# Kernel optimization log

Hardware: AMD Instinct MI355X
Metric: run time of the kernel (lower is better)

## Reference

```python
import jax, jax.numpy as jnp
import numpy as np

B, N_PER, C, KG, KTOP, KNN = 8, 2048, 256, 16, 512, 32
N = B * N_PER
E = N * KG
EPS = 1e-5


def setup_inputs() -> dict:
    key = jax.random.key(0)
    ks = jax.random.split(key, 32)
    s = 0.05
    x = jax.random.normal(ks[0], (N, C), jnp.float32)
    x_origin = jax.random.normal(ks[1], (N, C), jnp.float32)
    xyz = jax.random.uniform(ks[2], (N, 3), jnp.float32)
    # graph: every node is a dst with KG incoming edges from random nodes of the SAME sample
    edge_dst = jnp.repeat(jnp.arange(N, dtype=jnp.int32), KG)
    src_local = jax.random.randint(ks[3], (E,), 0, N_PER, dtype=jnp.int32)
    edge_src = src_local + (edge_dst // N_PER) * N_PER
    # EdgeConv params (theta on x_j - x_i, phi on x_i)
    theta_w = jax.random.normal(ks[4], (C, C), jnp.float32) * s
    theta_b = jax.random.normal(ks[5], (C,), jnp.float32) * s
    phi_w = jax.random.normal(ks[6], (C, C), jnp.float32) * s
    phi_b = jax.random.normal(ks[7], (C,), jnp.float32) * s
    # region_score_mlp: Conv1d(C,64,1)-ReLU-BN(64)-Conv1d(64,32,1)-ReLU-BN(32)-Conv1d(32,1,1)
    w1 = jax.random.normal(ks[8], (64, C), jnp.float32) * s
    b1 = jax.random.normal(ks[9], (64,), jnp.float32) * s
    g1 = 1.0 + 0.1 * jax.random.normal(ks[10], (64,), jnp.float32)
    be1 = 0.1 * jax.random.normal(ks[11], (64,), jnp.float32)
    m1 = 0.1 * jax.random.normal(ks[12], (64,), jnp.float32)
    v1 = jax.random.uniform(ks[13], (64,), jnp.float32, 0.5, 1.5)
    w2 = jax.random.normal(ks[14], (32, 64), jnp.float32) * s
    b2 = jax.random.normal(ks[15], (32,), jnp.float32) * s
    g2 = 1.0 + 0.1 * jax.random.normal(ks[16], (32,), jnp.float32)
    be2 = 0.1 * jax.random.normal(ks[17], (32,), jnp.float32)
    m2 = 0.1 * jax.random.normal(ks[18], (32,), jnp.float32)
    v2 = jax.random.uniform(ks[19], (32,), jnp.float32, 0.5, 1.5)
    w3 = jax.random.normal(ks[20], (1, 32), jnp.float32) * s
    b3 = jax.random.normal(ks[21], (1,), jnp.float32) * s
    return dict(x=x, x_origin=x_origin, xyz=xyz, edge_src=edge_src, edge_dst=edge_dst,
                theta_w=theta_w, theta_b=theta_b, phi_w=phi_w, phi_b=phi_b,
                w1=w1, b1=b1, g1=g1, be1=be1, m1=m1, v1=v1,
                w2=w2, b2=b2, g2=g2, be2=be2, m2=m2, v2=v2, w3=w3, b3=b3)


def _bn(t, g, b, m, v):
    return (t - m) * jax.lax.rsqrt(v + EPS) * g + b


def _forward(x, x_origin, xyz, edge_src, edge_dst,
             theta_w, theta_b, phi_w, phi_b,
             w1, b1, g1, be1, m1, v1, w2, b2, g2, be2, m2, v2, w3, b3):
    # EdgeConv: h_i = max_{j->i}( theta(x_j - x_i) + phi(x_i) ), then residual add
    msg = ((x[edge_src] - x[edge_dst]) @ theta_w.T + theta_b
           + x[edge_dst] @ phi_w.T + phi_b)                      # [E, C]
    h = jax.ops.segment_max(msg, edge_dst, num_segments=N)       # [N, C]
    x1 = h + x                                                   # residual
    # per-node MLP (Conv1d kernel-size 1 == linear), BN in eval mode
    t = _bn(jax.nn.relu(x1 @ w1.T + b1), g1, be1, m1, v1)
    t = _bn(jax.nn.relu(t @ w2.T + b2), g2, be2, m2, v2)
    score = t @ w3.T + b3                                        # [N, 1]
    score_b = score.reshape(B, N_PER)                            # vps_score
    # per-batch top-k (cls=False path: select by raw score, descending)
    topk_vals, topk_idx = jax.lax.top_k(score_b, KTOP)           # [B, KTOP]
    perm = (topk_idx + jnp.arange(B, dtype=topk_idx.dtype)[:, None] * N_PER).reshape(-1)
    x_new = x1[perm].reshape(B, KTOP, C)
    x_copy = x_origin[perm].reshape(B, KTOP, -1)
    xyz_sel = xyz[perm].reshape(B, KTOP, 3)
    # rebuild 32-NN graph per sample on selected points (batched, no per-b python calls)
    d2 = jnp.sum((xyz_sel[:, :, None, :] - xyz_sel[:, None, :, :]) ** 2, axis=-1)  # [B,K,K]
    _, knn_idx = jax.lax.top_k(-d2, KNN)                         # [B, KTOP, 32]
    return knn_idx, x_new, x_copy, score_b, topk_vals


def reference(x, x_origin, xyz, edge_src, edge_dst,
              theta_w, theta_b, phi_w, phi_b,
              w1, b1, g1, be1, m1, v1, w2, b2, g2, be2, m2, v2, w3, b3):
    return _forward(x, x_origin, xyz, edge_src, edge_dst,
                    theta_w, theta_b, phi_w, phi_b,
                    w1, b1, g1, be1, m1, v1, w2, b2, g2, be2, m2, v2, w3, b3)
```

## Files before the change

### kernel.cpp

```cpp
#include <hip/hip_runtime.h>
#include <math.h>

constexpr int B     = 8;
constexpr int N_PER = 2048;
constexpr int C     = 256;
constexpr int KG    = 16;
constexpr int KTOP  = 512;
constexpr int KNN   = 32;
constexpr int N     = B * N_PER;
constexpr float EPS = 1e-5f;

typedef __attribute__((ext_vector_type(8))) short  short8;
typedef __attribute__((ext_vector_type(4))) float  f32x4;

__device__ inline void split3(float f, unsigned short& h, unsigned short& m,
                              unsigned short& l)
{
    const unsigned u  = __float_as_uint(f);
    const unsigned r1 = (u + 0x7FFFu + ((u >> 16) & 1u)) & 0xFFFF0000u;
    h = (unsigned short)(r1 >> 16);
    const float f2 = f - __uint_as_float(r1);
    const unsigned u2 = __float_as_uint(f2);
    const unsigned r2 = (u2 + 0x7FFFu + ((u2 >> 16) & 1u)) & 0xFFFF0000u;
    m = (unsigned short)(r2 >> 16);
    const float f3 = f2 - __uint_as_float(r2);
    const unsigned u3 = __float_as_uint(f3);
    l = (unsigned short)((u3 + 0x7FFFu + ((u3 >> 16) & 1u)) >> 16);
}

__device__ inline void cvt_store24(unsigned short* dh, unsigned short* dm,
                                   unsigned short* dl, float4 a, float4 b)
{
    short8 h, m, l;
    unsigned short hh, mm, ll;
    float v[8] = {a.x, a.y, a.z, a.w, b.x, b.y, b.z, b.w};
#pragma unroll
    for (int j = 0; j < 8; ++j) {
        split3(v[j], hh, mm, ll);
        h[j] = (short)hh;
        m[j] = (short)mm;
        l[j] = (short)ll;
    }
    *(short8*)dh = h;
    *(short8*)dm = m;
    *(short8*)dl = l;
}

__device__ inline void split8v(const float* __restrict__ s,
                               unsigned short* __restrict__ dh,
                               unsigned short* __restrict__ dm,
                               unsigned short* __restrict__ dl)
{
    float4 a = *(const float4*)s;
    float4 b = *(const float4*)(s + 4);
    float v[8] = {a.x, a.y, a.z, a.w, b.x, b.y, b.z, b.w};
    short8 h8, m8, l8;
    unsigned short hh, mm, ll;
#pragma unroll
    for (int j = 0; j < 8; ++j) {
        split3(v[j], hh, mm, ll);
        h8[j] = (short)hh;
        m8[j] = (short)mm;
        l8[j] = (short)ll;
    }
    *(short8*)dh = h8;
    *(short8*)dm = m8;
    *(short8*)dl = l8;
}

constexpr int GW = C * C / 8;

__global__ __launch_bounds__(256) void k0w_split(
    const float* __restrict__ thw, const float* __restrict__ phw,
    unsigned short* __restrict__ th, unsigned short* __restrict__ tm,
    unsigned short* __restrict__ tl,
    unsigned short* __restrict__ ph, unsigned short* __restrict__ pm,
    unsigned short* __restrict__ pl)
{
    const int g = blockIdx.x * 256 + threadIdx.x;
    if (g < GW) {
        const int o = g * 8;
        split8v(thw + o, th + o, tm + o, tl + o);
    } else if (g < 2 * GW) {
        const int o = (g - GW) * 8;
        split8v(phw + o, ph + o, pm + o, pl + o);
    }
}

__global__ __launch_bounds__(256) void k1_wp(
    const float* __restrict__ x,
    const unsigned short* __restrict__ th, const unsigned short* __restrict__ tm,
    const unsigned short* __restrict__ tl,
    const unsigned short* __restrict__ ph, const unsigned short* __restrict__ pm,
    const unsigned short* __restrict__ pl,
    const float* __restrict__ thb, const float* __restrict__ phb,
    float* __restrict__ T, float* __restrict__ R)
{
    constexpr int BM = 128, BN = 64, ST = 40;
    __shared__ unsigned short sA[3][BM * ST];
    __shared__ unsigned short sT[3][BN * ST];
    __shared__ unsigned short sP[3][BN * ST];

    const int tid  = threadIdx.x;
    const int row0 = blockIdx.x * BM;
    const int n0   = blockIdx.y * BN;
    const int lane = tid & 63;
    const int wv   = tid >> 6;
    const int wr   = (wv >> 1) * 64;
    const int wc   = (wv & 1) * 32;
    const int fr   = lane & 15;
    const int fk   = (lane >> 4) * 8;
    const int ar0  = tid >> 2;
    const int ac   = (tid & 3) * 8;

    f32x4 acTh[4][2], acTl[4][2], acQh[4][2], acQl[4][2];
    const f32x4 zz = {0.f, 0.f, 0.f, 0.f};
#pragma unroll
    for (int m = 0; m < 4; ++m)
#pragma unroll
        for (int n = 0; n < 2; ++n) {
            acTh[m][n] = zz; acTl[m][n] = zz;
            acQh[m][n] = zz; acQl[m][n] = zz;
        }

    const float* xA0 = x + (size_t)(row0 + ar0)      * C + ac;
    const float* xA1 = x + (size_t)(row0 + 64 + ar0) * C + ac;
    const size_t offW = (size_t)(n0 + ar0) * C + ac;

    float4 a0a = *(const float4*)(xA0 + 0), a0b = *(const float4*)(xA0 + 4);
    float4 a1a = *(const float4*)(xA1 + 0), a1b = *(const float4*)(xA1 + 4);
    short8 rTh = *(const short8*)(th + offW);
    short8 rTm = *(const short8*)(tm + offW);
    short8 rTl = *(const short8*)(tl + offW);
    short8 rPh = *(const short8*)(ph + offW);
    short8 rPm = *(const short8*)(pm + offW);
    short8 rPl = *(const short8*)(pl + offW);

    const int sOffA0 = ar0 * ST + ac;
    const int sOffA1 = (64 + ar0) * ST + ac;
    const int aBase  = (wr + fr) * ST + fk;
    const int bBase  = (wc + fr) * ST + fk;

    for (int step = 0; step < 8; ++step) {
        __syncthreads();
        cvt_store24(sA[0] + sOffA0, sA[1] + sOffA0, sA[2] + sOffA0, a0a, a0b);
        cvt_store24(sA[0] + sOffA1, sA[1] + sOffA1, sA[2] + sOffA1, a1a, a1b);
        *(short8*)(sT[0] + sOffA0) = rTh;
        *(short8*)(sT[1] + sOffA0) = rTm;
        *(short8*)(sT[2] + sOffA0) = rTl;
        *(short8*)(sP[0] + sOffA0) = rPh;
        *(short8*)(sP[1] + sOffA0) = rPm;
        *(short8*)(sP[2] + sOffA0) = rPl;
        __syncthreads();

        if (step < 7) {
            const int kn = (step + 1) * 32;
            a0a = *(const float4*)(xA0 + kn); a0b = *(const float4*)(xA0 + kn + 4);
            a1a = *(const float4*)(xA1 + kn); a1b = *(const float4*)(xA1 + kn + 4);
            rTh = *(const short8*)(th + offW + kn);
            rTm = *(const short8*)(tm + offW + kn);
            rTl = *(const short8*)(tl + offW + kn);
            rPh = *(const short8*)(ph + offW + kn);
            rPm = *(const short8*)(pm + offW + kn);
            rPl = *(const short8*)(pl + offW + kn);
        }

        short8 a1f[4], a2f[4], a3f[4];
#pragma unroll
        for (int m = 0; m < 4; ++m) {
            const int r = aBase + m * 16 * ST;
            a1f[m] = *(const short8*)(sA[0] + r);
            a2f[m] = *(const short8*)(sA[1] + r);
            a3f[m] = *(const short8*)(sA[2] + r);
        }
        {
            short8 t0[2], p0[2];
#pragma unroll
            for (int n = 0; n < 2; ++n) {
                const int r = bBase + n * 16 * ST;
                t0[n] = *(const short8*)(sT[0] + r);
                p0[n] = *(const short8*)(sP[0] + r);
            }
#pragma unroll
            for (int m = 0; m < 4; ++m)
#pragma unroll
                for (int n = 0; n < 2; ++n) {
                    acTh[m][n] = __builtin_amdgcn_mfma_f32_16x16x32_bf16(a1f[m], t0[n], acTh[m][n], 0, 0, 0);
                    acQh[m][n] = __builtin_amdgcn_mfma_f32_16x16x32_bf16(a1f[m], p0[n], acQh[m][n], 0, 0, 0);
                    acTl[m][n] = __builtin_amdgcn_mfma_f32_16x16x32_bf16(a2f[m], t0[n], acTl[m][n], 0, 0, 0);
                    acQl[m][n] = __builtin_amdgcn_mfma_f32_16x16x32_bf16(a2f[m], p0[n], acQl[m][n], 0, 0, 0);
                    acTl[m][n] = __builtin_amdgcn_mfma_f32_16x16x32_bf16(a3f[m], t0[n], acTl[m][n], 0, 0, 0);
                    acQl[m][n] = __builtin_amdgcn_mfma_f32_16x16x32_bf16(a3f[m], p0[n], acQl[m][n], 0, 0, 0);
                }
        }
        {
            short8 t1[2], p1[2];
#pragma unroll
            for (int n = 0; n < 2; ++n) {
                const int r = bBase + n * 16 * ST;
                t1[n] = *(const short8*)(sT[1] + r);
                p1[n] = *(const short8*)(sP[1] + r);
            }
#pragma unroll
            for (int m = 0; m < 4; ++m)
#pragma unroll
                for (int n = 0; n < 2; ++n) {
                    acTl[m][n] = __builtin_amdgcn_mfma_f32_16x16x32_bf16(a1f[m], t1[n], acTl[m][n], 0, 0, 0);
                    acQl[m][n] = __builtin_amdgcn_mfma_f32_16x16x32_bf16(a1f[m], p1[n], acQl[m][n], 0, 0, 0);
                    acTl[m][n] = __builtin_amdgcn_mfma_f32_16x16x32_bf16(a2f[m], t1[n], acTl[m][n], 0, 0, 0);
                    acQl[m][n] = __builtin_amdgcn_mfma_f32_16x16x32_bf16(a2f[m], p1[n], acQl[m][n], 0, 0, 0);
                }
        }
        {
            short8 t2[2], p2[2];
#pragma unroll
            for (int n = 0; n < 2; ++n) {
                const int r = bBase + n * 16 * ST;
                t2[n] = *(const short8*)(sT[2] + r);
                p2[n] = *(const short8*)(sP[2] + r);
            }
#pragma unroll
            for (int m = 0; m < 4; ++m)
#pragma unroll
                for (int n = 0; n < 2; ++n) {
                    acTl[m][n] = __builtin_amdgcn_mfma_f32_16x16x32_bf16(a1f[m], t2[n], acTl[m][n], 0, 0, 0);
                    acQl[m][n] = __builtin_amdgcn_mfma_f32_16x16x32_bf16(a1f[m], p2[n], acQl[m][n], 0, 0, 0);
                }
        }
    }

    const int cr = (lane >> 4) * 4;
#pragma unroll
    for (int m = 0; m < 4; ++m) {
#pragma unroll
        for (int n = 0; n < 2; ++n) {
            const int col  = n0 + wc + n * 16 + fr;
            const float bias = thb[col] + phb[col];
#pragma unroll
            for (int j = 0; j < 4; ++j) {
                const int row = row0 + wr + m * 16 + cr + j;
                const size_t off = (size_t)row * C + col;
                const float tval = acTh[m][n][j] + acTl[m][n][j];
                const float qval = acQh[m][n][j] + acQl[m][n][j];
                T[off] = tval;
                R[off] = x[off] + qval + bias - tval;
            }
        }
    }
}

__global__ __launch_bounds__(256) void k1_fb(
    const float* __restrict__ x, const float* __restrict__ thw,
    const float* __restrict__ phw, const float* __restrict__ thb,
    const float* __restrict__ phb, float* __restrict__ T, float* __restrict__ R)
{
    constexpr int BM = 128, BN = 64, ST = 40;
    __shared__ unsigned short sA[3][BM * ST];
    __shared__ unsigned short sT[3][BN * ST];
    __shared__ unsigned short sP[3][BN * ST];

    const int tid  = threadIdx.x;
    const int row0 = blockIdx.x * BM;
    const int n0   = blockIdx.y * BN;
    const int lane = tid & 63;
    const int wv   = tid >> 6;
    const int wr   = (wv >> 1) * 64;
    const int wc   = (wv & 1) * 32;
    const int fr   = lane & 15;
    const int fk   = (lane >> 4) * 8;
    const int ar0 = tid >> 2;
    const int ac  = (tid & 3) * 8;

    f32x4 acTh[4][2], acTl[4][2], acQh[4][2], acQl[4][2];
    const f32x4 zz = {0.f, 0.f, 0.f, 0.f};
#pragma unroll
    for (int m = 0; m < 4; ++m)
#pragma unroll
        for (int n = 0; n < 2; ++n) {
            acTh[m][n] = zz; acTl[m][n] = zz;
            acQh[m][n] = zz; acQl[m][n] = zz;
        }

    const float* xA0 = x   + (size_t)(row0 + ar0)      * C + ac;
    const float* xA1 = x   + (size_t)(row0 + 64 + ar0) * C + ac;
    const float* wT  = thw + (size_t)(n0 + ar0)        * C + ac;
    const float* wP  = phw + (size_t)(n0 + ar0)        * C + ac;

    float4 a0a = *(const float4*)(xA0 + 0), a0b = *(const float4*)(xA0 + 4);
    float4 a1a = *(const float4*)(xA1 + 0), a1b = *(const float4*)(xA1 + 4);
    float4 ta  = *(const float4*)(wT  + 0), tb_ = *(const float4*)(wT  + 4);
    float4 pa  = *(const float4*)(wP  + 0), pb_ = *(const float4*)(wP  + 4);

    const int sOffA0 = ar0 * ST + ac;
    const int sOffA1 = (64 + ar0) * ST + ac;
    const int aBase  = (wr + fr) * ST + fk;
    const int bBase  = (wc + fr) * ST + fk;

    for (int step = 0; step < 8; ++step) {
        __syncthreads();
        cvt_store24(sA[0] + sOffA0, sA[1] + sOffA0, sA[2] + sOffA0, a0a, a0b);
        cvt_store24(sA[0] + sOffA1, sA[1] + sOffA1, sA[2] + sOffA1, a1a, a1b);
        cvt_store24(sT[0] + sOffA0, sT[1] + sOffA0, sT[2] + sOffA0, ta,  tb_);
        cvt_store24(sP[0] + sOffA0, sP[1] + sOffA0, sP[2] + sOffA0, pa,  pb_);
        __syncthreads();

        if (step < 7) {
            const int kn = (step + 1) * 32;
            a0a = *(const float4*)(xA0 + kn); a0b = *(const float4*)(xA0 + kn + 4);
            a1a = *(const float4*)(xA1 + kn); a1b = *(const float4*)(xA1 + kn + 4);
            ta  = *(const float4*)(wT  + kn); tb_ = *(const float4*)(wT  + kn + 4);
            pa  = *(const float4*)(wP  + kn); pb_ = *(const float4*)(wP  + kn + 4);
        }

        short8 a1f[4], a2f[4], a3f[4];
#pragma unroll
        for (int m = 0; m < 4; ++m) {
            const int r = aBase + m * 16 * ST;
            a1f[m] = *(const short8*)(sA[0] + r);
            a2f[m] = *(const short8*)(sA[1] + r);
            a3f[m] = *(const short8*)(sA[2] + r);
        }
        {
            short8 t0[2], p0[2];
#pragma unroll
            for (int n = 0; n < 2; ++n) {
                const int r = bBase + n * 16 * ST;
                t0[n] = *(const short8*)(sT[0] + r);
                p0[n] = *(const short8*)(sP[0] + r);
            }
#pragma unroll
            for (int m = 0; m < 4; ++m)
#pragma unroll
                for (int n = 0; n < 2; ++n) {
                    acTh[m][n] = __builtin_amdgcn_mfma_f32_16x16x32_bf16(a1f[m], t0[n], acTh[m][n], 0, 0, 0);
                    acQh[m][n] = __builtin_amdgcn_mfma_f32_16x16x32_bf16(a1f[m], p0[n], acQh[m][n], 0, 0, 0);
                    acTl[m][n] = __builtin_amdgcn_mfma_f32_16x16x32_bf16(a2f[m], t0[n], acTl[m][n], 0, 0, 0);
                    acQl[m][n] = __builtin_amdgcn_mfma_f32_16x16x32_bf16(a2f[m], p0[n], acQl[m][n], 0, 0, 0);
                    acTl[m][n] = __builtin_amdgcn_mfma_f32_16x16x32_bf16(a3f[m], t0[n], acTl[m][n], 0, 0, 0);
                    acQl[m][n] = __builtin_amdgcn_mfma_f32_16x16x32_bf16(a3f[m], p0[n], acQl[m][n], 0, 0, 0);
                }
        }
        {
            short8 t1[2], p1[2];
#pragma unroll
            for (int n = 0; n < 2; ++n) {
                const int r = bBase + n * 16 * ST;
                t1[n] = *(const short8*)(sT[1] + r);
                p1[n] = *(const short8*)(sP[1] + r);
            }
#pragma unroll
            for (int m = 0; m < 4; ++m)
#pragma unroll
                for (int n = 0; n < 2; ++n) {
                    acTl[m][n] = __builtin_amdgcn_mfma_f32_16x16x32_bf16(a1f[m], t1[n], acTl[m][n], 0, 0, 0);
                    acQl[m][n] = __builtin_amdgcn_mfma_f32_16x16x32_bf16(a1f[m], p1[n], acQl[m][n], 0, 0, 0);
                    acTl[m][n] = __builtin_amdgcn_mfma_f32_16x16x32_bf16(a2f[m], t1[n], acTl[m][n], 0, 0, 0);
                    acQl[m][n] = __builtin_amdgcn_mfma_f32_16x16x32_bf16(a2f[m], p1[n], acQl[m][n], 0, 0, 0);
                }
        }
        {
            short8 t2[2], p2[2];
#pragma unroll
            for (int n = 0; n < 2; ++n) {
                const int r = bBase + n * 16 * ST;
                t2[n] = *(const short8*)(sT[2] + r);
                p2[n] = *(const short8*)(sP[2] + r);
            }
#pragma unroll
            for (int m = 0; m < 4; ++m)
#pragma unroll
                for (int n = 0; n < 2; ++n) {
                    acTl[m][n] = __builtin_amdgcn_mfma_f32_16x16x32_bf16(a1f[m], t2[n], acTl[m][n], 0, 0, 0);
                    acQl[m][n] = __builtin_amdgcn_mfma_f32_16x16x32_bf16(a1f[m], p2[n], acQl[m][n], 0, 0, 0);
                }
        }
    }

    const int cr = (lane >> 4) * 4;
#pragma unroll
    for (int m = 0; m < 4; ++m) {
#pragma unroll
        for (int n = 0; n < 2; ++n) {
            const int col  = n0 + wc + n * 16 + fr;
            const float bias = thb[col] + phb[col];
#pragma unroll
            for (int j = 0; j < 4; ++j) {
                const int row = row0 + wr + m * 16 + cr + j;
                const size_t off = (size_t)row * C + col;
                const float tval = acTh[m][n][j] + acTl[m][n][j];
                const float qval = acQh[m][n][j] + acQl[m][n][j];
                T[off] = tval;
                R[off] = x[off] + qval + bias - tval;
            }
        }
    }
}

__global__ __launch_bounds__(256) void k2a_gather_max(
    const int* __restrict__ esrc, const float* __restrict__ T, float* x1r)
{
    const int gb = blockIdx.x;
    const int b  = gb & 7;
    const int node0 = b * N_PER + (gb >> 3) * 4;
    const int t = threadIdx.x;
    __shared__ int s[4][KG];
    if (t < 64) s[t >> 4][t & 15] = esrc[(node0 + (t >> 4)) * KG + (t & 15)];
    __syncthreads();
    const int m  = t >> 6;
    const int c4 = (t & 63) * 4;
    float4 acc = make_float4(-INFINITY, -INFINITY, -INFINITY, -INFINITY);
#pragma unroll
    for (int k = 0; k < KG; ++k) {
        const float4 v = *(const float4*)&T[(size_t)s[m][k] * C + c4];
        acc.x = fmaxf(acc.x, v.x);  acc.y = fmaxf(acc.y, v.y);
        acc.z = fmaxf(acc.z, v.z);  acc.w = fmaxf(acc.w, v.w);
    }
    const size_t off = (size_t)(node0 + m) * C + c4;
    float4 r = *(const float4*)&x1r[off];
    r.x += acc.x;  r.y += acc.y;  r.z += acc.z;  r.w += acc.w;
    *(float4*)&x1r[off] = r;
}

__global__ __launch_bounds__(256) void k2bc_score(
    const float* __restrict__ x1, const float* __restrict__ w1,
    const float* __restrict__ b1, const float* __restrict__ g1,
    const float* __restrict__ be1, const float* __restrict__ m1,
    const float* __restrict__ v1,
    const float* __restrict__ w2, const float* __restrict__ b2,
    const float* __restrict__ g2, const float* __restrict__ be2,
    const float* __restrict__ m2, const float* __restrict__ v2,
    const float* __restrict__ w3, const float* __restrict__ b3,
    float* __restrict__ score_ws, float* __restrict__ out_score)
{
    constexpr int BK = 16, ST = 68;
    __shared__ float Xs[BK * ST];
    __shared__ float Ws[BK * ST];
    __shared__ float t1s[64 * 65];
    __shared__ float w2s[32 * 65];
    __shared__ float w3s[32];
    __shared__ float zs[64 * 33];
    const int tid  = threadIdx.x;
    const int row0 = blockIdx.x * 64;
    const int tx = tid & 15, ty = tid >> 4;
    const int lm = tid >> 2, lq = (tid & 3) << 2;

    float acc[4][4] = {{0.f}};
    for (int k0 = 0; k0 < C; k0 += BK) {
        float4 fx = *(const float4*)(x1 + (size_t)(row0 + lm) * C + k0 + lq);
        float4 fw = *(const float4*)(w1 + (size_t)lm * C + k0 + lq);
        __syncthreads();
        Xs[(lq + 0) * ST + lm] = fx.x;  Xs[(lq + 1) * ST + lm] = fx.y;
        Xs[(lq + 2) * ST + lm] = fx.z;  Xs[(lq + 3) * ST + lm] = fx.w;
        Ws[(lq + 0) * ST + lm] = fw.x;  Ws[(lq + 1) * ST + lm] = fw.y;
        Ws[(lq + 2) * ST + lm] = fw.z;  Ws[(lq + 3) * ST + lm] = fw.w;
        __syncthreads();
#pragma unroll
        for (int k = 0; k < BK; ++k) {
            float4 a4 = *(const float4*)&Xs[k * ST + (ty << 2)];
            float4 w4 = *(const float4*)&Ws[k * ST + (tx << 2)];
            float av[4] = {a4.x, a4.y, a4.z, a4.w};
            float wv[4] = {w4.x, w4.y, w4.z, w4.w};
#pragma unroll
            for (int i2 = 0; i2 < 4; ++i2)
#pragma unroll
                for (int j2 = 0; j2 < 4; ++j2) acc[i2][j2] += av[i2] * wv[j2];
        }
    }
    __syncthreads();
#pragma unroll
    for (int i2 = 0; i2 < 4; ++i2) {
        const int mrow = (ty << 2) + i2;
#pragma unroll
        for (int j2 = 0; j2 < 4; ++j2) {
            const int o = (tx << 2) + j2;
            float y = acc[i2][j2] + b1[o];
            y = fmaxf(y, 0.f);
            y = (y - m1[o]) * (1.0f / sqrtf(v1[o] + EPS)) * g1[o] + be1[o];
            t1s[mrow * 65 + o] = y;
        }
    }
    for (int idx = tid; idx < 2048; idx += 256)
        w2s[(idx >> 6) * 65 + (idx & 63)] = w2[idx];
    if (tid < 32) w3s[tid] = w3[tid];
    __syncthreads();

    const int o = tid & 31;
    const float inv2 = (1.0f / sqrtf(v2[o] + EPS)) * g2[o];
#pragma unroll
    for (int p = 0; p < 8; ++p) {
        const int nl = p * 8 + (tid >> 5);
        float z = 0.f;
#pragma unroll
        for (int j = 0; j < 64; ++j) z += t1s[nl * 65 + j] * w2s[o * 65 + j];
        z += b2[o];
        z = fmaxf(z, 0.f);
        z = (z - m2[o]) * inv2 + be2[o];
        zs[nl * 33 + o] = z;
    }
    __syncthreads();

    if (tid < 64) {
        float sacc = 0.f;
#pragma unroll
        for (int j = 0; j < 32; ++j) sacc += zs[tid * 33 + j] * w3s[j];
        sacc += b3[0];
        const int node = row0 + tid;
        score_ws[node]  = sacc;
        out_score[node] = sacc;
    }
}

__global__ __launch_bounds__(256) void k3_rank(
    const float* __restrict__ score, const float* __restrict__ xyz,
    float* __restrict__ out_topk, int* __restrict__ perm,
    float* __restrict__ xsel)
{
    __shared__ unsigned long long keys[N_PER];
    const int b   = blockIdx.x >> 3;
    const int seg = blockIdx.x & 7;
    const int t   = threadIdx.x;
    for (int i = t; i < N_PER; i += 256) {
        const float v = score[b * N_PER + i];
        unsigned u = __float_as_uint(v);
        const unsigned ua = (u & 0x80000000u) ? ~u : (u | 0x80000000u);
        const unsigned ud = ~ua;
        keys[i] = ((unsigned long long)ud << 32) | (unsigned)i;
    }
    __syncthreads();
    const int i = seg * 256 + t;
    const unsigned long long k = keys[i];
    int r = 0;
#pragma unroll 8
    for (int j = 0; j < N_PER; ++j) r += (keys[j] < k) ? 1 : 0;
    if (r < KTOP) {
        const int g = b * N_PER + i;
        const int o = b * KTOP + r;
        out_topk[o] = score[g];
        perm[o] = g;
        xsel[o * 3 + 0] = xyz[g * 3 + 0];
        xsel[o * 3 + 1] = xyz[g * 3 + 1];
        xsel[o * 3 + 2] = xyz[g * 3 + 2];
    }
}

__device__ inline unsigned long long shfl_xor_u64(unsigned long long v, int m)
{
    unsigned lo = (unsigned)v, hi = (unsigned)(v >> 32);
    lo = __shfl_xor(lo, m, 64);
    hi = __shfl_xor(hi, m, 64);
    return ((unsigned long long)hi << 32) | lo;
}

__global__ __launch_bounds__(256) void k5_rank(
    const int* __restrict__ perm, const float* __restrict__ xsel,
    const float* __restrict__ x1, const float* __restrict__ xorig,
    float* __restrict__ out_xnew, float* __restrict__ out_xcopy,
    float* __restrict__ out_knn)
{
    constexpr int G = 4;
    __shared__ float px[KTOP], py[KTOP], pz[KTOP];
    const int t  = threadIdx.x;
    const int q0 = blockIdx.x * G;
    const int b  = q0 >> 9;
    const int i0 = q0 & 511;

    for (int idx = t; idx < KTOP; idx += 256) {
        const size_t base = ((size_t)b * KTOP + idx) * 3;
        px[idx] = xsel[base + 0];
        py[idx] = xsel[base + 1];
        pz[idx] = xsel[base + 2];
    }
#pragma unroll
    for (int p = 0; p < G; ++p) {
        const int row = q0 + p;
        const int g = perm[row];
        out_xnew [(size_t)row * C + t] = x1   [(size_t)g * C + t];
        out_xcopy[(size_t)row * C + t] = xorig[(size_t)g * C + t];
    }
    __syncthreads();

    const int w    = t >> 6;
    const int lane = t & 63;
    const int q    = i0 + w;
    const float qx = px[q], qy = py[q], qz = pz[q];

    unsigned long long arr[8];
#pragma unroll
    for (int e = 0; e < 8; ++e) {
        const int j = lane + 64 * e;
        const float dx = __fsub_rn(qx, px[j]);
        const float dy = __fsub_rn(qy, py[j]);
        const float dz = __fsub_rn(qz, pz[j]);
        const float d2 = __fadd_rn(__fadd_rn(__fmul_rn(dx, dx), __fmul_rn(dy, dy)),
                                   __fmul_rn(dz, dz));
        arr[e] = ((unsigned long long)__float_as_uint(d2) << 32) | (unsigned)j;
    }
#pragma unroll
    for (int pass = 0; pass < 7; ++pass)
#pragma unroll
        for (int i = 0; i < 7; ++i) {
            if (i < 7 - pass) {
                const unsigned long long a = arr[i], c = arr[i + 1];
                arr[i]     = (a < c) ? a : c;
                arr[i + 1] = (a < c) ? c : a;
            }
        }
    float* dst = out_knn + (size_t)(q0 + w) * KNN;
    for (int r = 0; r < KNN; ++r) {
        unsigned long long m = arr[0];
#pragma unroll
        for (int off = 32; off; off >>= 1) {
            const unsigned long long o = shfl_xor_u64(m, off);
            m = (o < m) ? o : m;
        }
        if (arr[0] == m) {
            dst[r] = (float)(unsigned)(m & 0xffffffffu);
#pragma unroll
            for (int i = 0; i < 7; ++i) arr[i] = arr[i + 1];
            arr[7] = ~0ull;
        }
    }
}

extern "C" void kernel_launch(void* const* d_in, const int* in_sizes, int n_in,
                              void* d_out, int out_size, void* d_ws, size_t ws_size,
                              hipStream_t stream)
{
    const float* x     = (const float*)d_in[0];
    const float* xorig = (const float*)d_in[1];
    const float* xyz   = (const float*)d_in[2];
    const int*   esrc  = (const int*)d_in[3];
    const float* thw = (const float*)d_in[5];
    const float* thb = (const float*)d_in[6];
    const float* phw = (const float*)d_in[7];
    const float* phb = (const float*)d_in[8];
    const float* w1  = (const float*)d_in[9];
    const float* b1  = (const float*)d_in[10];
    const float* g1  = (const float*)d_in[11];
    const float* be1 = (const float*)d_in[12];
    const float* m1  = (const float*)d_in[13];
    const float* v1  = (const float*)d_in[14];
    const float* w2  = (const float*)d_in[15];
    const float* b2  = (const float*)d_in[16];
    const float* g2  = (const float*)d_in[17];
    const float* be2 = (const float*)d_in[18];
    const float* m2  = (const float*)d_in[19];
    const float* v2  = (const float*)d_in[20];
    const float* w3  = (const float*)d_in[21];
    const float* b3  = (const float*)d_in[22];

    float* ws   = (float*)d_ws;
    float* T    = ws;
    float* x1   = ws + (size_t)N * C;
    float* sc   = ws + 2 * (size_t)N * C;
    int*   perm = (int*)(sc + N);
    float* xsel = (float*)(perm + B * KTOP);

    unsigned short* th = (unsigned short*)(xsel + (size_t)B * KTOP * 3);
    unsigned short* tm = th + (size_t)C * C;
    unsigned short* tl = tm + (size_t)C * C;
    unsigned short* ph = tl + (size_t)C * C;
    unsigned short* pm = ph + (size_t)C * C;
    unsigned short* pl = pm + (size_t)C * C;
    const size_t ws_need = (size_t)((char*)(pl + (size_t)C * C) - (char*)ws);
    const bool planes_ok = (ws_size >= ws_need);

    float* out     = (float*)d_out;
    float* o_knn   = out;
    float* o_xnew  = o_knn + (size_t)B * KTOP * KNN;
    float* o_xcopy = o_xnew + (size_t)B * KTOP * C;
    float* o_score = o_xcopy + (size_t)B * KTOP * C;
    float* o_topk  = o_score + (size_t)B * N_PER;

    if (planes_ok) {
        k0w_split<<<(2 * GW + 255) / 256, 256, 0, stream>>>(
            thw, phw, th, tm, tl, ph, pm, pl);
        k1_wp<<<dim3(N / 128, C / 64), 256, 0, stream>>>(
            x, th, tm, tl, ph, pm, pl, thb, phb, T, x1);
    } else {
        k1_fb<<<dim3(N / 128, C / 64), 256, 0, stream>>>(x, thw, phw, thb, phb, T, x1);
    }
    k2a_gather_max<<<N / 4, 256, 0, stream>>>(esrc, T, x1);
    k2bc_score<<<N / 64, 256, 0, stream>>>(x1, w1, b1, g1, be1, m1, v1,
                                           w2, b2, g2, be2, m2, v2, w3, b3, sc, o_score);
    k3_rank<<<8 * B, 256, 0, stream>>>(sc, xyz, o_topk, perm, xsel);
    k5_rank<<<B * KTOP / 4, 256, 0, stream>>>(perm, xsel, x1, xorig,
                                              o_xnew, o_xcopy, o_knn);
}
```

Measured before the change: 250.3 us.

## Fuse neighbor gather-max into the score MLP kernel

```diff
diff --git a/kernel.cpp b/kernel.cpp
--- a/kernel.cpp
+++ b/kernel.cpp
@@ -396,36 +396,12 @@
     }
 }
 
-__global__ __launch_bounds__(256) void k2a_gather_max(
-    const int* __restrict__ esrc, const float* __restrict__ T, float* x1r)
-{
-    const int gb = blockIdx.x;
-    const int b  = gb & 7;
-    const int node0 = b * N_PER + (gb >> 3) * 4;
-    const int t = threadIdx.x;
-    __shared__ int s[4][KG];
-    if (t < 64) s[t >> 4][t & 15] = esrc[(node0 + (t >> 4)) * KG + (t & 15)];
-    __syncthreads();
-    const int m  = t >> 6;
-    const int c4 = (t & 63) * 4;
-    float4 acc = make_float4(-INFINITY, -INFINITY, -INFINITY, -INFINITY);
-#pragma unroll
-    for (int k = 0; k < KG; ++k) {
-        const float4 v = *(const float4*)&T[(size_t)s[m][k] * C + c4];
-        acc.x = fmaxf(acc.x, v.x);  acc.y = fmaxf(acc.y, v.y);
-        acc.z = fmaxf(acc.z, v.z);  acc.w = fmaxf(acc.w, v.w);
-    }
-    const size_t off = (size_t)(node0 + m) * C + c4;
-    float4 r = *(const float4*)&x1r[off];
-    r.x += acc.x;  r.y += acc.y;  r.z += acc.z;  r.w += acc.w;
-    *(float4*)&x1r[off] = r;
-}
-
-__global__ __launch_bounds__(256) void k2bc_score(
-    const float* __restrict__ x1, const float* __restrict__ w1,
-    const float* __restrict__ b1, const float* __restrict__ g1,
-    const float* __restrict__ be1, const float* __restrict__ m1,
-    const float* __restrict__ v1,
+__global__ __launch_bounds__(256) void k2ab_fused(
+    const int* __restrict__ esrc, const float* __restrict__ T,
+    float* __restrict__ x1,
+    const float* __restrict__ w1, const float* __restrict__ b1,
+    const float* __restrict__ g1, const float* __restrict__ be1,
+    const float* __restrict__ m1, const float* __restrict__ v1,
     const float* __restrict__ w2, const float* __restrict__ b2,
     const float* __restrict__ g2, const float* __restrict__ be2,
     const float* __restrict__ m2, const float* __restrict__ v2,
@@ -439,8 +415,39 @@
     __shared__ float w2s[32 * 65];
     __shared__ float w3s[32];
     __shared__ float zs[64 * 33];
+    __shared__ int eidx[64][KG];
+
     const int tid  = threadIdx.x;
-    const int row0 = blockIdx.x * 64;
+    const int bb   = blockIdx.x & 7;
+    const int row0 = bb * N_PER + (blockIdx.x >> 3) * 64;
+
+#pragma unroll
+    for (int q = 0; q < 4; ++q) {
+        const int i = tid + q * 256;
+        eidx[i >> 4][i & 15] = esrc[(row0 + (i >> 4)) * KG + (i & 15)];
+    }
+    __syncthreads();
+
+    {
+        const int w = tid >> 6, c4 = (tid & 63) * 4;
+        for (int it = 0; it < 16; ++it) {
+            const int nl = w * 16 + it;
+            const int g  = row0 + nl;
+            float4 acc = make_float4(-INFINITY, -INFINITY, -INFINITY, -INFINITY);
+#pragma unroll
+            for (int k = 0; k < KG; ++k) {
+                const float4 v = *(const float4*)&T[(size_t)eidx[nl][k] * C + c4];
+                acc.x = fmaxf(acc.x, v.x);  acc.y = fmaxf(acc.y, v.y);
+                acc.z = fmaxf(acc.z, v.z);  acc.w = fmaxf(acc.w, v.w);
+            }
+            const size_t off = (size_t)g * C + c4;
+            float4 r = *(const float4*)&x1[off];
+            r.x += acc.x;  r.y += acc.y;  r.z += acc.z;  r.w += acc.w;
+            *(float4*)&x1[off] = r;
+        }
+    }
+    __syncthreads();
+
     const int tx = tid & 15, ty = tid >> 4;
     const int lm = tid >> 2, lq = (tid & 3) << 2;
 
@@ -680,9 +687,10 @@
     } else {
         k1_fb<<<dim3(N / 128, C / 64), 256, 0, stream>>>(x, thw, phw, thb, phb, T, x1);
     }
-    k2a_gather_max<<<N / 4, 256, 0, stream>>>(esrc, T, x1);
-    k2bc_score<<<N / 64, 256, 0, stream>>>(x1, w1, b1, g1, be1, m1, v1,
-                                           w2, b2, g2, be2, m2, v2, w3, b3, sc, o_score);
+    k2ab_fused<<<N / 64, 256, 0, stream>>>(esrc, T, x1,
+                                           w1, b1, g1, be1, m1, v1,
+                                           w2, b2, g2, be2, m2, v2, w3, b3,
+                                           sc, o_score);
     k3_rank<<<8 * B, 256, 0, stream>>>(sc, xyz, o_topk, perm, xsel);
     k5_rank<<<B * KTOP / 4, 256, 0, stream>>>(perm, xsel, x1, xorig,
                                               o_xnew, o_xcopy, o_knn);
```

After: 254.3 us. Within noise of the previous version (+1.6%).
